# Kernel optimization log

Measured on AMD Instinct MI355X. Metric: run time of the kernel, lower is better.

The kernel has to match this reference:

```python
import jax, jax.numpy as jnp
import numpy as np

ALPHA = 0.2  # LeakyReLU negative slope
NEG_INF = -9e15


def setup_inputs() -> dict:
    key = jax.random.key(0)
    k1, k2, k3, k4 = jax.random.split(key, 4)
    B, N, F_in, F_out = 8, 2048, 256, 128
    x = jax.random.normal(k1, (B, N, F_in), dtype=jnp.float32)
    adj = jax.random.randint(k2, (B, N, N), 0, 2, dtype=jnp.int32)
    # xavier-uniform-like init
    limW = float(np.sqrt(6.0 / (F_in + F_out)))
    W = jax.random.uniform(k3, (F_in, F_out), jnp.float32, -limW, limW)
    lima = float(np.sqrt(6.0 / (2 * F_out + 1)))
    a = jax.random.uniform(k4, (2 * F_out, 1), jnp.float32, -lima, lima)
    return {"x": x, "adj": adj, "W": W, "a": a}


def reference(x, adj, W, a):
    # x: [B, N, F_in], adj: [B, N, N], W: [F_in, F_out], a: [2*F_out, 1]
    F_out = W.shape[1]
    h = jnp.einsum('bnf,fo->bno', x, W)            # [B, N, F_out]
    a1 = a[:F_out, 0]                               # attends to source node i
    a2 = a[F_out:, 0]                               # attends to target node j
    f1 = h @ a1                                     # [B, N]
    f2 = h @ a2                                     # [B, N]
    # e[b,i,j] = leakyrelu(a1.h_i + a2.h_j) -- factored form of the concat trick
    e = jax.nn.leaky_relu(f1[:, :, None] + f2[:, None, :], negative_slope=ALPHA)
    attention = jnp.where(adj > 0, e, NEG_INF)
    attention = jax.nn.softmax(attention, axis=2)   # [B, N, N]
    # dropout is identity in eval mode
    h_prime = jnp.einsum('bij,bjo->bio', attention, h)  # [B, N, F_out]
    return jax.nn.elu(h_prime)                      # concat=True -> ELU
```

## Files before the change

### kernel.cpp

```cpp
#include <hip/hip_runtime.h>
#include <stdint.h>

#define BB   8
#define NN   2048
#define FIN  256
#define FOUT 128

using short8 = __attribute__((ext_vector_type(8))) short;
using f32x4  = __attribute__((ext_vector_type(4))) float;

__device__ __forceinline__ unsigned short rbf(float f) {
    return (unsigned short)((__float_as_uint(f) + 0x8000u) >> 16);
}

__device__ __forceinline__ void mfma_calib(int m, int quad, int* Mlab, int* Nlab) {
    short8 pa1, pb1, pa2, pb2;
    const short one = (short)0x3F80;
    const short mb  = (short)rbf((float)m);
#pragma unroll
    for (int j = 0; j < 8; ++j) { pa1[j] = 0; pa2[j] = 0; pb1[j] = mb; pb2[j] = one; }
    if (quad == 0) { pa1[0] = one; pa2[0] = mb; }
    f32x4 zz = {0.f, 0.f, 0.f, 0.f};
    f32x4 c1 = __builtin_amdgcn_mfma_f32_16x16x32_bf16(pa1, pb1, zz, 0, 0, 0);
    f32x4 c2 = __builtin_amdgcn_mfma_f32_16x16x32_bf16(pa2, pb2, zz, 0, 0, 0);
#pragma unroll
    for (int r = 0; r < 4; ++r) {
        Nlab[r] = ((int)c1[r]) & 15;
        Mlab[r] = ((int)c2[r]) & 15;
    }
}

__global__ __launch_bounds__(256) void gat_wt(const float* __restrict__ W,
                                              unsigned short* __restrict__ wt) {
    const int g  = blockIdx.x * 256 + threadIdx.x;
    const int k  = g >> 5;
    const int o4 = (g & 31) << 2;
    float4 wv = *(const float4*)(W + (k << 7) + o4);
    wt[((o4 + 0) << 8) + k] = rbf(wv.x);
    wt[((o4 + 1) << 8) + k] = rbf(wv.y);
    wt[((o4 + 2) << 8) + k] = rbf(wv.z);
    wt[((o4 + 3) << 8) + k] = rbf(wv.w);
}

__global__ __launch_bounds__(256) void gat_h3(
        const float* __restrict__ x, const unsigned short* __restrict__ wt,
        const float* __restrict__ a, unsigned short* __restrict__ ht,
        float* __restrict__ f1, float* __restrict__ f2) {
    __shared__ unsigned short xs[16][264];
    __shared__ float hs[16][132];
    const int bk   = blockIdx.x;
    const int R0   = bk << 4;
    const int b    = R0 >> 11;
    const int il0  = R0 & (NN - 1);
    const int tid  = threadIdx.x;
    const int w    = tid >> 6;
    const int lane = tid & 63;
    const int m    = lane & 15;
    const int quad = lane >> 4;

#pragma unroll
    for (int rr = 0; rr < 4; ++rr) {
        const int row = (w << 2) + rr;
        float4 xv = *(const float4*)(x + (size_t)(R0 + row) * FIN + (lane << 2));
        ushort4 c4;
        c4.x = rbf(xv.x); c4.y = rbf(xv.y); c4.z = rbf(xv.z); c4.w = rbf(xv.w);
        *(ushort4*)(&xs[row][lane << 2]) = c4;
    }
    int Mlab[4], Nlab[4];
    mfma_calib(m, quad, Mlab, Nlab);
    __syncthreads();

    f32x4 zz = {0.f, 0.f, 0.f, 0.f};
    f32x4 acc[2] = {zz, zz};
#pragma unroll
    for (int kc = 0; kc < 8; ++kc) {
        const int k0 = (kc << 5) + (quad << 3);
        short8 av = *(const short8*)(&xs[m][k0]);
#pragma unroll
        for (int t = 0; t < 2; ++t) {
            const int ot = (w << 1) + t;
            short8 bw = *(const short8*)(wt + (((ot << 4) + m) << 8) + k0);
            acc[t] = __builtin_amdgcn_mfma_f32_16x16x32_bf16(av, bw, acc[t], 0, 0, 0);
        }
    }
#pragma unroll
    for (int t = 0; t < 2; ++t)
#pragma unroll
        for (int r = 0; r < 4; ++r)
            hs[Mlab[r]][(((w << 1) + t) << 4) + Nlab[r]] = acc[t][r];
    __syncthreads();

    {
        const int i   = tid >> 4;
        const int seg = tid & 15;
        const int o0  = seg << 3;
        float s1 = 0.f, s2 = 0.f;
#pragma unroll
        for (int e = 0; e < 8; ++e) {
            float hv = hs[i][o0 + e];
            s1 = fmaf(hv, a[o0 + e], s1);
            s2 = fmaf(hv, a[FOUT + o0 + e], s2);
        }
        s1 += __shfl_xor(s1, 1); s1 += __shfl_xor(s1, 2);
        s1 += __shfl_xor(s1, 4); s1 += __shfl_xor(s1, 8);
        s2 += __shfl_xor(s2, 1); s2 += __shfl_xor(s2, 2);
        s2 += __shfl_xor(s2, 4); s2 += __shfl_xor(s2, 8);
        if (seg == 0) { f1[R0 + i] = s1; f2[R0 + i] = s2; }
    }
    {
        const int o  = tid >> 1;
        const int i8 = (tid & 1) << 3;
        short8 hv;
#pragma unroll
        for (int e = 0; e < 8; ++e) hv[e] = (short)rbf(hs[i8 + e][o]);
        *(short8*)(ht + ((size_t)((b << 7) + o) << 11) + il0 + i8) = hv;
    }
}

__global__ __launch_bounds__(256, 2) void gat_s4(
        const int* __restrict__ adj, const unsigned short* __restrict__ ht,
        const float* __restrict__ f1, const float* __restrict__ f2,
        float* __restrict__ out) {
    const int bk   = blockIdx.x;
    const int b    = bk & 7;
    const int i0   = (bk >> 3) << 5;
    const int tid  = threadIdx.x;
    const int w    = tid >> 6;
    const int lane = tid & 63;
    const int m    = lane & 15;
    const int quad = lane >> 4;

    __shared__ float accb[2][32][128];
    __shared__ float sbuf[4][2][16];

    int Mlab[4], Nlab[4];
    mfma_calib(m, quad, Mlab, Nlab);

    const int gi0 = (b << 11) + i0;
    const float f1a = f1[gi0 + m];
    const float f1b = f1[gi0 + 16 + m];
    const int* adjr0 = adj + ((size_t)(gi0 + m) << 11);
    const int* adjr1 = adj + ((size_t)(gi0 + 16 + m) << 11);
    const float* f2b = f2 + (b << 11);
    const unsigned short* htb = ht + ((size_t)b << 18);

    f32x4 zz = {0.f, 0.f, 0.f, 0.f};
    f32x4 acc1[8], acc2[8];
#pragma unroll
    for (int t = 0; t < 8; ++t) { acc1[t] = zz; acc2[t] = zz; }
    float s1 = 0.f, s2 = 0.f;

    const int jb = (w << 9) + (quad << 3);
#pragma unroll 2
    for (int c = 0; c < 16; ++c) {
        const int j0 = jb + (c << 5);
        short8 hf[8];
#pragma unroll
        for (int ot = 0; ot < 8; ++ot)
            hf[ot] = *(const short8*)(htb + ((size_t)((ot << 4) + m) << 11) + j0);

        int4   aA0 = *(const int4*)(adjr0 + j0);
        int4   aA1 = *(const int4*)(adjr0 + j0 + 4);
        int4   aB0 = *(const int4*)(adjr1 + j0);
        int4   aB1 = *(const int4*)(adjr1 + j0 + 4);
        float4 fa  = *(const float4*)(f2b + j0);
        float4 fb  = *(const float4*)(f2b + j0 + 4);
        float fm[8] = {fa.x, fa.y, fa.z, fa.w, fb.x, fb.y, fb.z, fb.w};

        float pA[8], pB[8];
        {
            int am[8] = {aA0.x, aA0.y, aA0.z, aA0.w, aA1.x, aA1.y, aA1.z, aA1.w};
#pragma unroll
            for (int u = 0; u < 8; ++u) {
                float e = f1a + fm[u];
                pA[u] = (am[u] > 0) ? __expf(fmaxf(e, 0.2f * e)) : 0.f;
            }
        }
        {
            int bm[8] = {aB0.x, aB0.y, aB0.z, aB0.w, aB1.x, aB1.y, aB1.z, aB1.w};
#pragma unroll
            for (int u = 0; u < 8; ++u) {
                float e = f1b + fm[u];
                pB[u] = (bm[u] > 0) ? __expf(fmaxf(e, 0.2f * e)) : 0.f;
            }
        }
        s1 += ((pA[0] + pA[1]) + (pA[2] + pA[3])) + ((pA[4] + pA[5]) + (pA[6] + pA[7]));
        s2 += ((pB[0] + pB[1]) + (pB[2] + pB[3])) + ((pB[4] + pB[5]) + (pB[6] + pB[7]));

        short8 pf1, pf2;
#pragma unroll
        for (int u = 0; u < 8; ++u) { pf1[u] = (short)rbf(pA[u]); pf2[u] = (short)rbf(pB[u]); }

#pragma unroll
        for (int ot = 0; ot < 8; ++ot) {
            acc1[ot] = __builtin_amdgcn_mfma_f32_16x16x32_bf16(pf1, hf[ot], acc1[ot], 0, 0, 0);
            acc2[ot] = __builtin_amdgcn_mfma_f32_16x16x32_bf16(pf2, hf[ot], acc2[ot], 0, 0, 0);
        }
    }

    s1 += __shfl_xor(s1, 16); s1 += __shfl_xor(s1, 32);
    s2 += __shfl_xor(s2, 16); s2 += __shfl_xor(s2, 32);
    if (lane < 16) { sbuf[w][0][lane] = s1; sbuf[w][1][lane] = s2; }

    if (w < 2) {
#pragma unroll
        for (int ot = 0; ot < 8; ++ot)
#pragma unroll
            for (int r = 0; r < 4; ++r) {
                accb[w][Mlab[r]][(ot << 4) + Nlab[r]]      = acc1[ot][r];
                accb[w][16 + Mlab[r]][(ot << 4) + Nlab[r]] = acc2[ot][r];
            }
    }
    __syncthreads();
    if (w >= 2) {
#pragma unroll
        for (int ot = 0; ot < 8; ++ot)
#pragma unroll
            for (int r = 0; r < 4; ++r) {
                accb[w - 2][Mlab[r]][(ot << 4) + Nlab[r]]      += acc1[ot][r];
                accb[w - 2][16 + Mlab[r]][(ot << 4) + Nlab[r]] += acc2[ot][r];
            }
    }
    __syncthreads();

    {
        const int row = tid >> 3;
        const int o0  = (tid & 7) << 4;
        const int g   = row >> 4;
        const int mm  = row & 15;
        const float s = (sbuf[0][g][mm] + sbuf[1][g][mm]) +
                        (sbuf[2][g][mm] + sbuf[3][g][mm]);
        const float inv = 1.0f / s;
        float* orow = out + (((size_t)gi0 + row) << 7) + o0;
#pragma unroll
        for (int v4 = 0; v4 < 4; ++v4) {
            float4 rv;
            float y;
            y = (accb[0][row][o0 + 4 * v4 + 0] + accb[1][row][o0 + 4 * v4 + 0]) * inv;
            rv.x = y > 0.f ? y : expm1f(y);
            y = (accb[0][row][o0 + 4 * v4 + 1] + accb[1][row][o0 + 4 * v4 + 1]) * inv;
            rv.y = y > 0.f ? y : expm1f(y);
            y = (accb[0][row][o0 + 4 * v4 + 2] + accb[1][row][o0 + 4 * v4 + 2]) * inv;
            rv.z = y > 0.f ? y : expm1f(y);
            y = (accb[0][row][o0 + 4 * v4 + 3] + accb[1][row][o0 + 4 * v4 + 3]) * inv;
            rv.w = y > 0.f ? y : expm1f(y);
            *(float4*)(orow + 4 * v4) = rv;
        }
    }
}

extern "C" void kernel_launch(void* const* d_in, const int* in_sizes, int n_in,
                              void* d_out, int out_size, void* d_ws, size_t ws_size,
                              hipStream_t stream) {
    const float* x   = nullptr;
    const int*   adj = nullptr;
    const float* W   = nullptr;
    const float* a   = nullptr;
    for (int i = 0; i < n_in; ++i) {
        const long s = in_sizes[i];
        if      (s == (long)BB * NN * NN)  adj = (const int*)d_in[i];
        else if (s == (long)BB * NN * FIN) x   = (const float*)d_in[i];
        else if (s == (long)FIN * FOUT)    W   = (const float*)d_in[i];
        else if (s == 2L * FOUT)           a   = (const float*)d_in[i];
    }
    if (!x)   x   = (const float*)d_in[0];
    if (!adj) adj = (const int*)d_in[1];
    if (!W)   W   = (const float*)d_in[2];
    if (!a)   a   = (const float*)d_in[3];
    float* out = (float*)d_out;

    unsigned short* wt = (unsigned short*)d_ws;
    unsigned short* ht = wt + 32768;
    float* f1 = (float*)(ht + (size_t)BB * NN * FOUT);
    float* f2 = f1 + BB * NN;

    hipLaunchKernelGGL(gat_wt, dim3(32),   dim3(256), 0, stream, W, wt);
    hipLaunchKernelGGL(gat_h3, dim3(1024), dim3(256), 0, stream, x, wt, a, ht, f1, f2);
    hipLaunchKernelGGL(gat_s4, dim3(512),  dim3(256), 0, stream, adj, ht, f1, f2, out);
}
```

Before: 247.1 us.

## Split attention kernel j-range across eight waves per block

The attention-aggregation kernel moves from 256 to 512 threads per block. Eight waves each cover a 256-column slice of j instead of four waves covering 512, which halves the serial loop length per wave and raises the number of waves in flight. The cross-wave reduction is reorganised to fit the same shared-memory budget: the two 16-row accumulator halves are reduced and written out one after the other, which adds extra barriers and LDS traffic. The launch bounds request 4 blocks per CU, which may force register spilling given the 64 accumulator floats plus 8 short8 fragments held per thread.

After: 355.9 us. +44.0%, slower.

```diff
diff --git a/kernel.cpp b/kernel.cpp
--- a/kernel.cpp
+++ b/kernel.cpp
@@ -117,7 +117,7 @@
     }
 }
 
-__global__ __launch_bounds__(256, 2) void gat_s4(
+__global__ __launch_bounds__(512, 4) void gat_s8(
         const int* __restrict__ adj, const unsigned short* __restrict__ ht,
         const float* __restrict__ f1, const float* __restrict__ f2,
         float* __restrict__ out) {
@@ -130,8 +130,8 @@
     const int m    = lane & 15;
     const int quad = lane >> 4;
 
-    __shared__ float accb[2][32][128];
-    __shared__ float sbuf[4][2][16];
+    __shared__ float accb[4][16][128];
+    __shared__ float sbuf[8][2][16];
 
     int Mlab[4], Nlab[4];
     mfma_calib(m, quad, Mlab, Nlab);
@@ -150,9 +150,9 @@
     for (int t = 0; t < 8; ++t) { acc1[t] = zz; acc2[t] = zz; }
     float s1 = 0.f, s2 = 0.f;
 
-    const int jb = (w << 9) + (quad << 3);
+    const int jb = (w << 8) + (quad << 3);
 #pragma unroll 2
-    for (int c = 0; c < 16; ++c) {
+    for (int c = 0; c < 8; ++c) {
         const int j0 = jb + (c << 5);
         short8 hf[8];
 #pragma unroll
@@ -202,50 +202,77 @@
     s2 += __shfl_xor(s2, 16); s2 += __shfl_xor(s2, 32);
     if (lane < 16) { sbuf[w][0][lane] = s1; sbuf[w][1][lane] = s2; }
 
-    if (w < 2) {
-#pragma unroll
-        for (int ot = 0; ot < 8; ++ot)
-#pragma unroll
-            for (int r = 0; r < 4; ++r) {
-                accb[w][Mlab[r]][(ot << 4) + Nlab[r]]      = acc1[ot][r];
-                accb[w][16 + Mlab[r]][(ot << 4) + Nlab[r]] = acc2[ot][r];
-            }
-    }
-    __syncthreads();
-    if (w >= 2) {
-#pragma unroll
-        for (int ot = 0; ot < 8; ++ot)
-#pragma unroll
-            for (int r = 0; r < 4; ++r) {
-                accb[w - 2][Mlab[r]][(ot << 4) + Nlab[r]]      += acc1[ot][r];
-                accb[w - 2][16 + Mlab[r]][(ot << 4) + Nlab[r]] += acc2[ot][r];
-            }
-    }
-    __syncthreads();
-
+    if (w < 4) {
+#pragma unroll
+        for (int ot = 0; ot < 8; ++ot)
+#pragma unroll
+            for (int r = 0; r < 4; ++r)
+                accb[w][Mlab[r]][(ot << 4) + Nlab[r]] = acc1[ot][r];
+    }
+    __syncthreads();
+    if (w >= 4) {
+#pragma unroll
+        for (int ot = 0; ot < 8; ++ot)
+#pragma unroll
+            for (int r = 0; r < 4; ++r)
+                accb[w - 4][Mlab[r]][(ot << 4) + Nlab[r]] += acc1[ot][r];
+    }
+    __syncthreads();
     {
-        const int row = tid >> 3;
-        const int o0  = (tid & 7) << 4;
-        const int g   = row >> 4;
-        const int mm  = row & 15;
-        const float s = (sbuf[0][g][mm] + sbuf[1][g][mm]) +
-                        (sbuf[2][g][mm] + sbuf[3][g][mm]);
+        const int row = tid >> 5;
+        const int o0  = (tid & 31) << 2;
+        const float s = ((sbuf[0][0][row] + sbuf[1][0][row]) + (sbuf[2][0][row] + sbuf[3][0][row]))
+                      + ((sbuf[4][0][row] + sbuf[5][0][row]) + (sbuf[6][0][row] + sbuf[7][0][row]));
         const float inv = 1.0f / s;
         float* orow = out + (((size_t)gi0 + row) << 7) + o0;
-#pragma unroll
-        for (int v4 = 0; v4 < 4; ++v4) {
-            float4 rv;
-            float y;
-            y = (accb[0][row][o0 + 4 * v4 + 0] + accb[1][row][o0 + 4 * v4 + 0]) * inv;
-            rv.x = y > 0.f ? y : expm1f(y);
-            y = (accb[0][row][o0 + 4 * v4 + 1] + accb[1][row][o0 + 4 * v4 + 1]) * inv;
-            rv.y = y > 0.f ? y : expm1f(y);
-            y = (accb[0][row][o0 + 4 * v4 + 2] + accb[1][row][o0 + 4 * v4 + 2]) * inv;
-            rv.z = y > 0.f ? y : expm1f(y);
-            y = (accb[0][row][o0 + 4 * v4 + 3] + accb[1][row][o0 + 4 * v4 + 3]) * inv;
-            rv.w = y > 0.f ? y : expm1f(y);
-            *(float4*)(orow + 4 * v4) = rv;
-        }
+        float4 rv;
+        float y;
+        y = (accb[0][row][o0 + 0] + accb[1][row][o0 + 0] + accb[2][row][o0 + 0] + accb[3][row][o0 + 0]) * inv;
+        rv.x = y > 0.f ? y : expm1f(y);
+        y = (accb[0][row][o0 + 1] + accb[1][row][o0 + 1] + accb[2][row][o0 + 1] + accb[3][row][o0 + 1]) * inv;
+        rv.y = y > 0.f ? y : expm1f(y);
+        y = (accb[0][row][o0 + 2] + accb[1][row][o0 + 2] + accb[2][row][o0 + 2] + accb[3][row][o0 + 2]) * inv;
+        rv.z = y > 0.f ? y : expm1f(y);
+        y = (accb[0][row][o0 + 3] + accb[1][row][o0 + 3] + accb[2][row][o0 + 3] + accb[3][row][o0 + 3]) * inv;
+        rv.w = y > 0.f ? y : expm1f(y);
+        *(float4*)orow = rv;
+    }
+    __syncthreads();
+
+    if (w < 4) {
+#pragma unroll
+        for (int ot = 0; ot < 8; ++ot)
+#pragma unroll
+            for (int r = 0; r < 4; ++r)
+                accb[w][Mlab[r]][(ot << 4) + Nlab[r]] = acc2[ot][r];
+    }
+    __syncthreads();
+    if (w >= 4) {
+#pragma unroll
+        for (int ot = 0; ot < 8; ++ot)
+#pragma unroll
+            for (int r = 0; r < 4; ++r)
+                accb[w - 4][Mlab[r]][(ot << 4) + Nlab[r]] += acc2[ot][r];
+    }
+    __syncthreads();
+    {
+        const int row = tid >> 5;
+        const int o0  = (tid & 31) << 2;
+        const float s = ((sbuf[0][1][row] + sbuf[1][1][row]) + (sbuf[2][1][row] + sbuf[3][1][row]))
+                      + ((sbuf[4][1][row] + sbuf[5][1][row]) + (sbuf[6][1][row] + sbuf[7][1][row]));
+        const float inv = 1.0f / s;
+        float* orow = out + (((size_t)gi0 + 16 + row) << 7) + o0;
+        float4 rv;
+        float y;
+        y = (accb[0][row][o0 + 0] + accb[1][row][o0 + 0] + accb[2][row][o0 + 0] + accb[3][row][o0 + 0]) * inv;
+        rv.x = y > 0.f ? y : expm1f(y);
+        y = (accb[0][row][o0 + 1] + accb[1][row][o0 + 1] + accb[2][row][o0 + 1] + accb[3][row][o0 + 1]) * inv;
+        rv.y = y > 0.f ? y : expm1f(y);
+        y = (accb[0][row][o0 + 2] + accb[1][row][o0 + 2] + accb[2][row][o0 + 2] + accb[3][row][o0 + 2]) * inv;
+        rv.z = y > 0.f ? y : expm1f(y);
+        y = (accb[0][row][o0 + 3] + accb[1][row][o0 + 3] + accb[2][row][o0 + 3] + accb[3][row][o0 + 3]) * inv;
+        rv.w = y > 0.f ? y : expm1f(y);
+        *(float4*)orow = rv;
     }
 }
 
@@ -276,5 +303,5 @@
 
     hipLaunchKernelGGL(gat_wt, dim3(32),   dim3(256), 0, stream, W, wt);
     hipLaunchKernelGGL(gat_h3, dim3(1024), dim3(256), 0, stream, x, wt, a, ht, f1, f2);
-    hipLaunchKernelGGL(gat_s4, dim3(512),  dim3(256), 0, stream, adj, ht, f1, f2, out);
-}
+    hipLaunchKernelGGL(gat_s8, dim3(512),  dim3(512), 0, stream, adj, ht, f1, f2, out);
+}
```

## Shrink attention row tile to 16 rows per block and double the grid

Applied to the files above, without the earlier changes.

The attention kernel now handles 16 query rows per block instead of 32, so it launches twice as many blocks and needs half the accumulator registers. Launch bounds are raised to 4 blocks per SIMD to improve occupancy and latency hiding on the adjacency stream. The cross-wave reduction becomes a single shared-memory pass over four padded slices, which removes one barrier. In exchange, each loaded ht fragment feeds half as many MFMAs, so total ht traffic from L2 doubles.

Result: slower. 277.0 us (+12.1%).

```diff
diff --git a/kernel.cpp b/kernel.cpp
--- a/kernel.cpp
+++ b/kernel.cpp
@@ -117,38 +117,33 @@
     }
 }
 
-__global__ __launch_bounds__(256, 2) void gat_s4(
+__global__ __launch_bounds__(256, 4) void gat_s16(
         const int* __restrict__ adj, const unsigned short* __restrict__ ht,
         const float* __restrict__ f1, const float* __restrict__ f2,
         float* __restrict__ out) {
     const int bk   = blockIdx.x;
     const int b    = bk & 7;
-    const int i0   = (bk >> 3) << 5;
+    const int i0   = (bk >> 3) << 4;
     const int tid  = threadIdx.x;
     const int w    = tid >> 6;
     const int lane = tid & 63;
     const int m    = lane & 15;
     const int quad = lane >> 4;
 
-    __shared__ float accb[2][32][128];
-    __shared__ float sbuf[4][2][16];
-
-    int Mlab[4], Nlab[4];
-    mfma_calib(m, quad, Mlab, Nlab);
+    __shared__ float accb[4][16][130];
+    __shared__ float sbuf[4][16];
 
     const int gi0 = (b << 11) + i0;
     const float f1a = f1[gi0 + m];
-    const float f1b = f1[gi0 + 16 + m];
     const int* adjr0 = adj + ((size_t)(gi0 + m) << 11);
-    const int* adjr1 = adj + ((size_t)(gi0 + 16 + m) << 11);
     const float* f2b = f2 + (b << 11);
     const unsigned short* htb = ht + ((size_t)b << 18);
 
     f32x4 zz = {0.f, 0.f, 0.f, 0.f};
-    f32x4 acc1[8], acc2[8];
-#pragma unroll
-    for (int t = 0; t < 8; ++t) { acc1[t] = zz; acc2[t] = zz; }
-    float s1 = 0.f, s2 = 0.f;
+    f32x4 acc[8];
+#pragma unroll
+    for (int t = 0; t < 8; ++t) acc[t] = zz;
+    float s1 = 0.f;
 
     const int jb = (w << 9) + (quad << 3);
 #pragma unroll 2
@@ -161,13 +156,11 @@
 
         int4   aA0 = *(const int4*)(adjr0 + j0);
         int4   aA1 = *(const int4*)(adjr0 + j0 + 4);
-        int4   aB0 = *(const int4*)(adjr1 + j0);
-        int4   aB1 = *(const int4*)(adjr1 + j0 + 4);
         float4 fa  = *(const float4*)(f2b + j0);
         float4 fb  = *(const float4*)(f2b + j0 + 4);
         float fm[8] = {fa.x, fa.y, fa.z, fa.w, fb.x, fb.y, fb.z, fb.w};
 
-        float pA[8], pB[8];
+        float pA[8];
         {
             int am[8] = {aA0.x, aA0.y, aA0.z, aA0.w, aA1.x, aA1.y, aA1.z, aA1.w};
 #pragma unroll
@@ -176,75 +169,50 @@
                 pA[u] = (am[u] > 0) ? __expf(fmaxf(e, 0.2f * e)) : 0.f;
             }
         }
-        {
-            int bm[8] = {aB0.x, aB0.y, aB0.z, aB0.w, aB1.x, aB1.y, aB1.z, aB1.w};
-#pragma unroll
-            for (int u = 0; u < 8; ++u) {
-                float e = f1b + fm[u];
-                pB[u] = (bm[u] > 0) ? __expf(fmaxf(e, 0.2f * e)) : 0.f;
-            }
-        }
         s1 += ((pA[0] + pA[1]) + (pA[2] + pA[3])) + ((pA[4] + pA[5]) + (pA[6] + pA[7]));
-        s2 += ((pB[0] + pB[1]) + (pB[2] + pB[3])) + ((pB[4] + pB[5]) + (pB[6] + pB[7]));
-
-        short8 pf1, pf2;
-#pragma unroll
-        for (int u = 0; u < 8; ++u) { pf1[u] = (short)rbf(pA[u]); pf2[u] = (short)rbf(pB[u]); }
-
-#pragma unroll
-        for (int ot = 0; ot < 8; ++ot) {
-            acc1[ot] = __builtin_amdgcn_mfma_f32_16x16x32_bf16(pf1, hf[ot], acc1[ot], 0, 0, 0);
-            acc2[ot] = __builtin_amdgcn_mfma_f32_16x16x32_bf16(pf2, hf[ot], acc2[ot], 0, 0, 0);
-        }
+
+        short8 pf1;
+#pragma unroll
+        for (int u = 0; u < 8; ++u) pf1[u] = (short)rbf(pA[u]);
+
+#pragma unroll
+        for (int ot = 0; ot < 8; ++ot)
+            acc[ot] = __builtin_amdgcn_mfma_f32_16x16x32_bf16(pf1, hf[ot], acc[ot], 0, 0, 0);
     }
 
     s1 += __shfl_xor(s1, 16); s1 += __shfl_xor(s1, 32);
-    s2 += __shfl_xor(s2, 16); s2 += __shfl_xor(s2, 32);
-    if (lane < 16) { sbuf[w][0][lane] = s1; sbuf[w][1][lane] = s2; }
-
-    if (w < 2) {
-#pragma unroll
-        for (int ot = 0; ot < 8; ++ot)
-#pragma unroll
-            for (int r = 0; r < 4; ++r) {
-                accb[w][Mlab[r]][(ot << 4) + Nlab[r]]      = acc1[ot][r];
-                accb[w][16 + Mlab[r]][(ot << 4) + Nlab[r]] = acc2[ot][r];
-            }
-    }
+    if (lane < 16) sbuf[w][lane] = s1;
+
+    int Mlab[4], Nlab[4];
+    mfma_calib(m, quad, Mlab, Nlab);
+
+#pragma unroll
+    for (int ot = 0; ot < 8; ++ot)
+#pragma unroll
+        for (int r = 0; r < 4; ++r)
+            accb[w][Mlab[r]][(ot << 4) + Nlab[r]] = acc[ot][r];
     __syncthreads();
-    if (w >= 2) {
-#pragma unroll
-        for (int ot = 0; ot < 8; ++ot)
-#pragma unroll
-            for (int r = 0; r < 4; ++r) {
-                accb[w - 2][Mlab[r]][(ot << 4) + Nlab[r]]      += acc1[ot][r];
-                accb[w - 2][16 + Mlab[r]][(ot << 4) + Nlab[r]] += acc2[ot][r];
-            }
-    }
-    __syncthreads();
 
     {
-        const int row = tid >> 3;
-        const int o0  = (tid & 7) << 4;
-        const int g   = row >> 4;
-        const int mm  = row & 15;
-        const float s = (sbuf[0][g][mm] + sbuf[1][g][mm]) +
-                        (sbuf[2][g][mm] + sbuf[3][g][mm]);
+        const int row = tid >> 4;
+        const int o0  = (tid & 15) << 3;
+        const float s = (sbuf[0][row] + sbuf[1][row]) + (sbuf[2][row] + sbuf[3][row]);
         const float inv = 1.0f / s;
         float* orow = out + (((size_t)gi0 + row) << 7) + o0;
 #pragma unroll
-        for (int v4 = 0; v4 < 4; ++v4) {
+        for (int v4 = 0; v4 < 2; ++v4) {
             float4 rv;
             float y;
-            y = (accb[0][row][o0 + 4 * v4 + 0] + accb[1][row][o0 + 4 * v4 + 0]) * inv;
+            const int oo = o0 + (v4 << 2);
+            y = (accb[0][row][oo + 0] + accb[1][row][oo + 0] + accb[2][row][oo + 0] + accb[3][row][oo + 0]) * inv;
             rv.x = y > 0.f ? y : expm1f(y);
-            y = (accb[0][row][o0 + 4 * v4 + 1] + accb[1][row][o0 + 4 * v4 + 1]) * inv;
+            y = (accb[0][row][oo + 1] + accb[1][row][oo + 1] + accb[2][row][oo + 1] + accb[3][row][oo + 1]) * inv;
             rv.y = y > 0.f ? y : expm1f(y);
-            y = (accb[0][row][o0 + 4 * v4 + 2] + accb[1][row][o0 + 4 * v4 + 2]) * inv;
+            y = (accb[0][row][oo + 2] + accb[1][row][oo + 2] + accb[2][row][oo + 2] + accb[3][row][oo + 2]) * inv;
             rv.z = y > 0.f ? y : expm1f(y);
-            y = (accb[0][row][o0 + 4 * v4 + 3] + accb[1][row][o0 + 4 * v4 + 3]) * inv;
+            y = (accb[0][row][oo + 3] + accb[1][row][oo + 3] + accb[2][row][oo + 3] + accb[3][row][oo + 3]) * inv;
             rv.w = y > 0.f ? y : expm1f(y);
-            *(float4*)(orow + 4 * v4) = rv;
+            *(float4*)(orow + (v4 << 2)) = rv;
         }
     }
 }
@@ -274,7 +242,7 @@
     float* f1 = (float*)(ht + (size_t)BB * NN * FOUT);
     float* f2 = f1 + BB * NN;
 
-    hipLaunchKernelGGL(gat_wt, dim3(32),   dim3(256), 0, stream, W, wt);
-    hipLaunchKernelGGL(gat_h3, dim3(1024), dim3(256), 0, stream, x, wt, a, ht, f1, f2);
-    hipLaunchKernelGGL(gat_s4, dim3(512),  dim3(256), 0, stream, adj, ht, f1, f2, out);
-}
+    hipLaunchKernelGGL(gat_wt,  dim3(32),   dim3(256), 0, stream, W, wt);
+    hipLaunchKernelGGL(gat_h3,  dim3(1024), dim3(256), 0, stream, x, wt, a, ht, f1, f2);
+    hipLaunchKernelGGL(gat_s16, dim3(1024), dim3(256), 0, stream, adj, ht, f1, f2, out);
+}
```

## Split attention aggregation over neighbour halves with a separate finalize kernel

Applied to the files above, without the earlier changes.

The attention/aggregation kernel now processes only half of the neighbour range per block, doubling the grid to 1024 blocks, and raises the launch-bound occupancy target to 4. Partial weighted sums and partial softmax denominators are written to workspace, and a new kernel combines the two halves, normalises, and applies ELU. This aims to improve latency hiding and CU fill, at the cost of extra workspace traffic, an extra launch, and possible register pressure from the higher occupancy bound.

Result: slower. 362.0 us (+46.5%).

```diff
diff --git a/kernel.cpp b/kernel.cpp
--- a/kernel.cpp
+++ b/kernel.cpp
@@ -117,13 +117,14 @@
     }
 }
 
-__global__ __launch_bounds__(256, 2) void gat_s4(
+__global__ __launch_bounds__(256, 4) void gat_s2a(
         const int* __restrict__ adj, const unsigned short* __restrict__ ht,
         const float* __restrict__ f1, const float* __restrict__ f2,
-        float* __restrict__ out) {
+        float* __restrict__ wsp, float* __restrict__ wss) {
     const int bk   = blockIdx.x;
     const int b    = bk & 7;
-    const int i0   = (bk >> 3) << 5;
+    const int jh   = (bk >> 3) & 1;
+    const int i0   = (bk >> 4) << 5;
     const int tid  = threadIdx.x;
     const int w    = tid >> 6;
     const int lane = tid & 63;
@@ -150,9 +151,9 @@
     for (int t = 0; t < 8; ++t) { acc1[t] = zz; acc2[t] = zz; }
     float s1 = 0.f, s2 = 0.f;
 
-    const int jb = (w << 9) + (quad << 3);
+    const int jb = (jh << 10) + (w << 8) + (quad << 3);
 #pragma unroll 2
-    for (int c = 0; c < 16; ++c) {
+    for (int c = 0; c < 8; ++c) {
         const int j0 = jb + (c << 5);
         short8 hf[8];
 #pragma unroll
@@ -226,27 +227,42 @@
     {
         const int row = tid >> 3;
         const int o0  = (tid & 7) << 4;
-        const int g   = row >> 4;
-        const int mm  = row & 15;
+        float* prow = wsp + ((size_t)jh << 21) + (((size_t)gi0 + row) << 7) + o0;
+#pragma unroll
+        for (int v4 = 0; v4 < 4; ++v4) {
+            float4 rv;
+            rv.x = accb[0][row][o0 + 4 * v4 + 0] + accb[1][row][o0 + 4 * v4 + 0];
+            rv.y = accb[0][row][o0 + 4 * v4 + 1] + accb[1][row][o0 + 4 * v4 + 1];
+            rv.z = accb[0][row][o0 + 4 * v4 + 2] + accb[1][row][o0 + 4 * v4 + 2];
+            rv.w = accb[0][row][o0 + 4 * v4 + 3] + accb[1][row][o0 + 4 * v4 + 3];
+            *(float4*)(prow + 4 * v4) = rv;
+        }
+    }
+    if (tid < 32) {
+        const int g  = tid >> 4;
+        const int mm = tid & 15;
         const float s = (sbuf[0][g][mm] + sbuf[1][g][mm]) +
                         (sbuf[2][g][mm] + sbuf[3][g][mm]);
-        const float inv = 1.0f / s;
-        float* orow = out + (((size_t)gi0 + row) << 7) + o0;
-#pragma unroll
-        for (int v4 = 0; v4 < 4; ++v4) {
-            float4 rv;
-            float y;
-            y = (accb[0][row][o0 + 4 * v4 + 0] + accb[1][row][o0 + 4 * v4 + 0]) * inv;
-            rv.x = y > 0.f ? y : expm1f(y);
-            y = (accb[0][row][o0 + 4 * v4 + 1] + accb[1][row][o0 + 4 * v4 + 1]) * inv;
-            rv.y = y > 0.f ? y : expm1f(y);
-            y = (accb[0][row][o0 + 4 * v4 + 2] + accb[1][row][o0 + 4 * v4 + 2]) * inv;
-            rv.z = y > 0.f ? y : expm1f(y);
-            y = (accb[0][row][o0 + 4 * v4 + 3] + accb[1][row][o0 + 4 * v4 + 3]) * inv;
-            rv.w = y > 0.f ? y : expm1f(y);
-            *(float4*)(orow + 4 * v4) = rv;
-        }
-    }
+        wss[(jh << 14) + gi0 + tid] = s;
+    }
+}
+
+__global__ __launch_bounds__(256) void gat_fin(
+        const float* __restrict__ wsp, const float* __restrict__ wss,
+        float* __restrict__ out) {
+    const int g4 = blockIdx.x * 256 + threadIdx.x;
+    const int gi = g4 >> 5;
+    const float s   = wss[gi] + wss[(1 << 14) + gi];
+    const float inv = 1.0f / s;
+    float4 p0 = *(const float4*)(wsp + ((size_t)g4 << 2));
+    float4 p1 = *(const float4*)(wsp + (1u << 21) + ((size_t)g4 << 2));
+    float4 rv;
+    float y;
+    y = (p0.x + p1.x) * inv; rv.x = y > 0.f ? y : expm1f(y);
+    y = (p0.y + p1.y) * inv; rv.y = y > 0.f ? y : expm1f(y);
+    y = (p0.z + p1.z) * inv; rv.z = y > 0.f ? y : expm1f(y);
+    y = (p0.w + p1.w) * inv; rv.w = y > 0.f ? y : expm1f(y);
+    *(float4*)(out + ((size_t)g4 << 2)) = rv;
 }
 
 extern "C" void kernel_launch(void* const* d_in, const int* in_sizes, int n_in,
@@ -271,10 +287,13 @@
 
     unsigned short* wt = (unsigned short*)d_ws;
     unsigned short* ht = wt + 32768;
-    float* f1 = (float*)(ht + (size_t)BB * NN * FOUT);
-    float* f2 = f1 + BB * NN;
-
-    hipLaunchKernelGGL(gat_wt, dim3(32),   dim3(256), 0, stream, W, wt);
-    hipLaunchKernelGGL(gat_h3, dim3(1024), dim3(256), 0, stream, x, wt, a, ht, f1, f2);
-    hipLaunchKernelGGL(gat_s4, dim3(512),  dim3(256), 0, stream, adj, ht, f1, f2, out);
-}
+    float* f1  = (float*)(ht + (size_t)BB * NN * FOUT);
+    float* f2  = f1 + BB * NN;
+    float* wss = f2 + BB * NN;
+    float* wsp = wss + 2 * BB * NN;
+
+    hipLaunchKernelGGL(gat_wt,  dim3(32),   dim3(256), 0, stream, W, wt);
+    hipLaunchKernelGGL(gat_h3,  dim3(1024), dim3(256), 0, stream, x, wt, a, ht, f1, f2);
+    hipLaunchKernelGGL(gat_s2a, dim3(1024), dim3(256), 0, stream, adj, ht, f1, f2, wsp, wss);
+    hipLaunchKernelGGL(gat_fin, dim3(2048), dim3(256), 0, stream, wsp, wss, out);
+}
```
